# Optimization experiments

Measured on AMD Instinct MI355X. Metric: run time of the kernel, lower is better.

The kernel has to match this reference:

```python
import jax, jax.numpy as jnp
import numpy as np

TEMP = 0.1  # self._get_temperature


def _gate(cur_iter):
    return max((10000 - cur_iter) / 10000.0, 0.0)


def _vector_quantize(feat, codebook, gate):
    # feat: (b, c, h, w), codebook: (k, c)
    b, c, h, w = feat.shape
    flat = feat.transpose(0, 2, 3, 1).reshape(-1, c)  # (N, c)
    distance = (jnp.sum(flat * flat, axis=1, keepdims=True)
                + jnp.sum(codebook * codebook, axis=1)
                - 2.0 * jnp.matmul(flat, codebook.T))  # (N, k)
    prob = jax.nn.softmax(-distance / TEMP, axis=-1)  # (N, k)
    assignment = prob.reshape(b, h, w, -1).transpose(0, 3, 1, 2)  # (b, k, h, w)
    q_feat = jnp.matmul(prob, codebook).reshape(b, h, w, c).transpose(0, 3, 1, 2)
    out_feat = feat * gate + q_feat * (1.0 - gate)
    return out_feat, assignment, distance


def _head(x, w1, b1, w2, b2):
    # two 1x1 convs with ReLU in between
    y = jnp.einsum('bchw,oc->bohw', x, w1) + b1[None, :, None, None]
    y = jax.nn.relu(y)
    y = jnp.einsum('bchw,oc->bohw', y, w2) + b2[None, :, None, None]
    return y


def setup_inputs() -> dict:
    key = jax.random.key(0)
    ks = jax.random.split(key, 6)
    B, C, H, W = 32, 64, 40, 40
    K0, C1 = 2048, 256
    K1 = 512
    return {
        'x0': jax.random.normal(ks[0], (B, C, H, W), dtype=jnp.float32),
        'vq0': jax.random.normal(ks[1], (K0, C), dtype=jnp.float32),
        'vq1': jax.random.normal(ks[2], (K1, C1), dtype=jnp.float32),
        'head_w1': jax.random.normal(ks[3], (C1, C), dtype=jnp.float32) * 0.05,
        'head_b1': jnp.zeros((C1,), dtype=jnp.float32),
        'head_w2': jax.random.normal(ks[4], (C1, C1), dtype=jnp.float32) * 0.05,
        'head_b2': jnp.zeros((C1,), dtype=jnp.float32),
        'cur_iter': 5000,
    }


def reference(x0, vq0, vq1, head_w1, head_b1, head_w2, head_b2, cur_iter):
    gate = _gate(cur_iter)
    qx0, a0, d0 = _vector_quantize(x0, vq0, gate)
    x3 = _head(qx0, head_w1, head_b1, head_w2, head_b2)
    qx3, a3, d3 = _vector_quantize(x3, vq1, gate)
    # mirrors torch forward return: ([x0, x3], [qx0, qx3], [a0, a3], [d0, d3])
    return (x3, qx0, qx3, a0, a3, d0, d3)
```

## Files before the change

kernel.cpp:

```cpp
#include <hip/hip_runtime.h>
#include <math.h>

#define HW   1600
#define C0   64
#define K0   2048
#define C1   256
#define K1   512

static const size_t OFF_X3  = 0;
static const size_t OFF_QX0 = 13107200;
static const size_t OFF_QX3 = 16384000;
static const size_t OFF_A0  = 29491200;
static const size_t OFF_A3  = 134348800;
static const size_t OFF_D0  = 160563200;
static const size_t OFF_D3  = 265420800;

__global__ __launch_bounds__(256) void k_esq(const float* __restrict__ vq0,
                                             const float* __restrict__ vq1,
                                             float* __restrict__ esq) {
    int r = blockIdx.x * 256 + threadIdx.x;
    if (r < K0) {
        float s = 0.f;
        for (int c = 0; c < C0; c++) { float v = vq0[r * C0 + c]; s += v * v; }
        esq[r] = s;
    } else if (r < K0 + K1) {
        int rr = r - K0;
        float s = 0.f;
        for (int c = 0; c < C1; c++) { float v = vq1[rr * C1 + c]; s += v * v; }
        esq[K0 + rr] = s;
    }
}

__global__ __launch_bounds__(256) void k_dist0(const float* __restrict__ x0,
                                               const float* __restrict__ cb,
                                               const float* __restrict__ esq,
                                               float* __restrict__ d0,
                                               float* __restrict__ stats) {
    __shared__ __align__(16) float xs[32][68];
    __shared__ float xsq[32];
    __shared__ __align__(16) float esT[64][132];
    __shared__ float rowM[32], rowS[32];

    const int t = threadIdx.x;
    const int n0 = blockIdx.x * 32;
    const int b = n0 / HW, hw0 = n0 % HW;

    for (int i = t; i < 32 * 64; i += 256) {
        int c = i >> 5, r = i & 31;
        xs[r][c] = x0[(size_t)(b * C0 + c) * HW + hw0 + r];
    }
    __syncthreads();
    if (t < 32) {
        float s = 0.f;
        for (int c = 0; c < 64; c++) { float v = xs[t][c]; s += v * v; }
        xsq[t] = s; rowM[t] = -1e30f; rowS[t] = 0.f;
    }
    __syncthreads();

    const int rg = t >> 5;
    const int kg = t & 31;

    for (int k0 = 0; k0 < K0; k0 += 128) {
        for (int i = t; i < 128 * 64; i += 256) {
            int c = i & 63, kk = i >> 6;
            esT[c][kk] = cb[(size_t)(k0 + kk) * C0 + c];
        }
        __syncthreads();

        float acc[4][4];
        #pragma unroll
        for (int i = 0; i < 4; i++)
            #pragma unroll
            for (int j = 0; j < 4; j++) acc[i][j] = 0.f;

        #pragma unroll 2
        for (int c = 0; c < 64; c += 4) {
            float xv[4][4];
            #pragma unroll
            for (int i = 0; i < 4; i++) {
                float4 xt = *(const float4*)&xs[rg * 4 + i][c];
                xv[i][0] = xt.x; xv[i][1] = xt.y; xv[i][2] = xt.z; xv[i][3] = xt.w;
            }
            #pragma unroll
            for (int q = 0; q < 4; q++) {
                float4 ev = *(const float4*)&esT[c + q][kg * 4];
                #pragma unroll
                for (int i = 0; i < 4; i++) {
                    acc[i][0] += xv[i][q] * ev.x;
                    acc[i][1] += xv[i][q] * ev.y;
                    acc[i][2] += xv[i][q] * ev.z;
                    acc[i][3] += xv[i][q] * ev.w;
                }
            }
        }

        float4 eq = *(const float4*)&esq[k0 + kg * 4];
        float eqv[4] = {eq.x, eq.y, eq.z, eq.w};
        float mrow[4], srow[4];
        #pragma unroll
        for (int i = 0; i < 4; i++) {
            int r = rg * 4 + i;
            float xq = xsq[r];
            float dv[4];
            #pragma unroll
            for (int j = 0; j < 4; j++) dv[j] = xq + eqv[j] - 2.f * acc[i][j];
            float4 st; st.x = dv[0]; st.y = dv[1]; st.z = dv[2]; st.w = dv[3];
            *(float4*)&d0[(size_t)(n0 + r) * K0 + k0 + kg * 4] = st;
            float m = -10.f * dv[0];
            m = fmaxf(m, -10.f * dv[1]);
            m = fmaxf(m, -10.f * dv[2]);
            m = fmaxf(m, -10.f * dv[3]);
            float s = 0.f;
            #pragma unroll
            for (int j = 0; j < 4; j++) s += __expf(-10.f * dv[j] - m);
            mrow[i] = m; srow[i] = s;
        }
        #pragma unroll
        for (int off = 1; off < 32; off <<= 1) {
            #pragma unroll
            for (int i = 0; i < 4; i++) {
                float m2 = __shfl_xor(mrow[i], off, 64);
                float s2 = __shfl_xor(srow[i], off, 64);
                float M = fmaxf(mrow[i], m2);
                srow[i] = srow[i] * __expf(mrow[i] - M) + s2 * __expf(m2 - M);
                mrow[i] = M;
            }
        }
        if (kg == 0) {
            #pragma unroll
            for (int i = 0; i < 4; i++) {
                int r = rg * 4 + i;
                float Mo = rowM[r], So = rowS[r];
                float M = fmaxf(Mo, mrow[i]);
                rowS[r] = So * __expf(Mo - M) + srow[i] * __expf(mrow[i] - M);
                rowM[r] = M;
            }
        }
        __syncthreads();
    }
    if (t < 32) {
        stats[(size_t)(n0 + t) * 2]     = rowM[t];
        stats[(size_t)(n0 + t) * 2 + 1] = rowS[t];
    }
}

__global__ __launch_bounds__(256) void k_prob0(const float* __restrict__ x0,
                                               const float* __restrict__ cb,
                                               const float* __restrict__ stats,
                                               const int* __restrict__ iter,
                                               const float* __restrict__ d0,
                                               float* __restrict__ out) {
    __shared__ __align__(16) float es[128][68];
    __shared__ float ptT[128][33];
    __shared__ float rowMv[32], rowIS[32];

    const int t = threadIdx.x;
    const int n0 = blockIdx.x * 32;
    const int b = n0 / HW, hw0 = n0 % HW;

    if (t < 32) {
        rowMv[t] = stats[(size_t)(n0 + t) * 2];
        rowIS[t] = 1.f / stats[(size_t)(n0 + t) * 2 + 1];
    }
    __syncthreads();

    const int r1 = t >> 3;
    const int ks1 = (t & 7) * 16;
    const int rq = t & 31;
    const int cg = t >> 5;
    const float Mr1 = rowMv[r1], IS1 = rowIS[r1];

    float qf[8];
    #pragma unroll
    for (int q = 0; q < 8; q++) qf[q] = 0.f;

    float* a0 = out + OFF_A0;

    for (int k0 = 0; k0 < K0; k0 += 128) {
        for (int i = t; i < 128 * 64; i += 256) {
            int kk = i >> 6, c = i & 63;
            es[kk][c] = cb[(size_t)(k0 + kk) * C0 + c];
        }
        const float* dr = &d0[(size_t)(n0 + r1) * K0 + k0 + ks1];
        #pragma unroll
        for (int q = 0; q < 4; q++) {
            float4 dv = *(const float4*)&dr[q * 4];
            ptT[ks1 + q * 4 + 0][r1] = __expf(-10.f * dv.x - Mr1) * IS1;
            ptT[ks1 + q * 4 + 1][r1] = __expf(-10.f * dv.y - Mr1) * IS1;
            ptT[ks1 + q * 4 + 2][r1] = __expf(-10.f * dv.z - Mr1) * IS1;
            ptT[ks1 + q * 4 + 3][r1] = __expf(-10.f * dv.w - Mr1) * IS1;
        }
        __syncthreads();
        #pragma unroll
        for (int jj = 0; jj < 16; jj++) {
            int pos = jj * 256 + t;
            int kk = pos >> 5, r = pos & 31;
            a0[(size_t)(b * K0 + k0 + kk) * HW + hw0 + r] = ptT[kk][r];
        }
        #pragma unroll 8
        for (int kk = 0; kk < 128; kk++) {
            float p = ptT[kk][rq];
            float4 e0 = *(const float4*)&es[kk][cg * 8];
            float4 e1 = *(const float4*)&es[kk][cg * 8 + 4];
            qf[0] += p * e0.x; qf[1] += p * e0.y; qf[2] += p * e0.z; qf[3] += p * e0.w;
            qf[4] += p * e1.x; qf[5] += p * e1.y; qf[6] += p * e1.z; qf[7] += p * e1.w;
        }
        __syncthreads();
    }
    float gate = fmaxf((10000.f - (float)(*iter)) / 10000.f, 0.f);
    float om = 1.f - gate;
    #pragma unroll
    for (int q = 0; q < 8; q++) {
        int c = cg * 8 + q;
        size_t idx = (size_t)(b * C0 + c) * HW + hw0 + rq;
        out[OFF_QX0 + idx] = gate * x0[idx] + om * qf[q];
    }
}

__global__ __launch_bounds__(256) void k_head(const float* __restrict__ w1,
                                              const float* __restrict__ b1,
                                              const float* __restrict__ w2,
                                              const float* __restrict__ b2,
                                              float* __restrict__ out) {
    __shared__ __align__(16) float xin[32][64];
    __shared__ __align__(16) float y1s[32][256];
    __shared__ __align__(16) float wst[64][68];

    const int t = threadIdx.x;
    const int n0 = blockIdx.x * 32;
    const int b = n0 / HW, hw0 = n0 % HW;
    const float* qx0 = out + OFF_QX0;
    float* x3 = out + OFF_X3;

    for (int i = t; i < 32 * 64; i += 256) {
        int c = i >> 5, r = i & 31;
        xin[r][c] = qx0[(size_t)(b * C0 + c) * HW + hw0 + r];
    }
    __syncthreads();

    const int rg = t >> 5;
    const int og = t & 31;

    for (int op = 0; op < 4; op++) {
        int ob = op * 64;
        for (int i = t; i < 64 * 64; i += 256) {
            int c = i & 63, o = i >> 6;
            wst[c][o] = w1[(size_t)(ob + o) * C0 + c];
        }
        __syncthreads();
        float2 bb = *(const float2*)&b1[ob + og * 2];
        float acc[4][2];
        #pragma unroll
        for (int i = 0; i < 4; i++) { acc[i][0] = bb.x; acc[i][1] = bb.y; }
        #pragma unroll 2
        for (int c = 0; c < 64; c += 4) {
            float xv[4][4];
            #pragma unroll
            for (int i = 0; i < 4; i++) {
                float4 xt = *(const float4*)&xin[rg * 4 + i][c];
                xv[i][0] = xt.x; xv[i][1] = xt.y; xv[i][2] = xt.z; xv[i][3] = xt.w;
            }
            #pragma unroll
            for (int q = 0; q < 4; q++) {
                float2 wv = *(const float2*)&wst[c + q][og * 2];
                #pragma unroll
                for (int i = 0; i < 4; i++) {
                    acc[i][0] += xv[i][q] * wv.x;
                    acc[i][1] += xv[i][q] * wv.y;
                }
            }
        }
        #pragma unroll
        for (int i = 0; i < 4; i++) {
            float2 st;
            st.x = fmaxf(acc[i][0], 0.f);
            st.y = fmaxf(acc[i][1], 0.f);
            *(float2*)&y1s[rg * 4 + i][ob + og * 2] = st;
        }
        __syncthreads();
    }

    for (int p = 0; p < 4; p++) {
        int ob = p * 64;
        float2 bb = *(const float2*)&b2[ob + og * 2];
        float acc[4][2];
        #pragma unroll
        for (int i = 0; i < 4; i++) { acc[i][0] = bb.x; acc[i][1] = bb.y; }
        for (int cc0 = 0; cc0 < 256; cc0 += 64) {
            for (int i = t; i < 64 * 64; i += 256) {
                int c = i & 63, o = i >> 6;
                wst[c][o] = w2[(size_t)(ob + o) * C1 + cc0 + c];
            }
            __syncthreads();
            #pragma unroll 2
            for (int c = 0; c < 64; c += 4) {
                float yv[4][4];
                #pragma unroll
                for (int i = 0; i < 4; i++) {
                    float4 yt = *(const float4*)&y1s[rg * 4 + i][cc0 + c];
                    yv[i][0] = yt.x; yv[i][1] = yt.y; yv[i][2] = yt.z; yv[i][3] = yt.w;
                }
                #pragma unroll
                for (int q = 0; q < 4; q++) {
                    float2 wv = *(const float2*)&wst[c + q][og * 2];
                    #pragma unroll
                    for (int i = 0; i < 4; i++) {
                        acc[i][0] += yv[i][q] * wv.x;
                        acc[i][1] += yv[i][q] * wv.y;
                    }
                }
            }
            __syncthreads();
        }
        #pragma unroll
        for (int i = 0; i < 4; i++)
            *(float2*)&wst[0][0 + (size_t)(rg * 4 + i) * 68 + og * 2] =
                make_float2(acc[i][0], acc[i][1]);
        __syncthreads();
        for (int i = t; i < 32 * 64; i += 256) {
            int o = i >> 5, r = i & 31;
            x3[(size_t)(b * C1 + ob + o) * HW + hw0 + r] = wst[0][(size_t)r * 68 + o];
        }
        __syncthreads();
    }
}

__global__ __launch_bounds__(256) void k_dist1(const float* __restrict__ cb,
                                               const float* __restrict__ esq,
                                               const float* __restrict__ x3,
                                               float* __restrict__ d3,
                                               float* __restrict__ stats) {
    __shared__ __align__(16) float xs[32][132];
    __shared__ float esT[128][33];
    __shared__ float xsq[32];
    __shared__ float part[32][8];
    __shared__ float rowM[32], rowS[32];

    const int t = threadIdx.x;
    const int n0 = blockIdx.x * 32;
    const int b = n0 / HW, hw0 = n0 % HW;

    {
        int r = t & 31, seg = t >> 5;
        float s = 0.f;
        for (int j = 0; j < 32; j++) {
            float v = x3[(size_t)(b * C1 + seg * 32 + j) * HW + hw0 + r];
            s += v * v;
        }
        part[r][seg] = s;
    }
    __syncthreads();
    if (t < 32) {
        float s = 0.f;
        for (int j = 0; j < 8; j++) s += part[t][j];
        xsq[t] = s; rowM[t] = -1e30f; rowS[t] = 0.f;
    }
    __syncthreads();

    const int rg = t >> 5;
    const int kg = t & 31;

    for (int k0 = 0; k0 < K1; k0 += 32) {
        float acc[4] = {0.f, 0.f, 0.f, 0.f};
        for (int ch = 0; ch < 2; ch++) {
            for (int i = t; i < 32 * 128; i += 256) {
                int c = i & 127, kk = i >> 7;
                esT[c][kk] = cb[(size_t)(k0 + kk) * C1 + ch * 128 + c];
            }
            for (int i = t; i < 32 * 128; i += 256) {
                int ci = i >> 5, r = i & 31;
                xs[r][ci] = x3[(size_t)(b * C1 + ch * 128 + ci) * HW + hw0 + r];
            }
            __syncthreads();
            #pragma unroll 2
            for (int c = 0; c < 128; c += 4) {
                float ev[4];
                #pragma unroll
                for (int q = 0; q < 4; q++) ev[q] = esT[c + q][kg];
                #pragma unroll
                for (int i = 0; i < 4; i++) {
                    float4 xt = *(const float4*)&xs[rg * 4 + i][c];
                    acc[i] += xt.x * ev[0] + xt.y * ev[1] + xt.z * ev[2] + xt.w * ev[3];
                }
            }
            __syncthreads();
        }
        float eqv = esq[k0 + kg];
        float mrow[4], srow[4];
        #pragma unroll
        for (int i = 0; i < 4; i++) {
            int r = rg * 4 + i;
            float dv = xsq[r] + eqv - 2.f * acc[i];
            d3[(size_t)(n0 + r) * K1 + k0 + kg] = dv;
            mrow[i] = -10.f * dv; srow[i] = 1.f;
        }
        #pragma unroll
        for (int off = 1; off < 32; off <<= 1) {
            #pragma unroll
            for (int i = 0; i < 4; i++) {
                float m2 = __shfl_xor(mrow[i], off, 64);
                float s2 = __shfl_xor(srow[i], off, 64);
                float M = fmaxf(mrow[i], m2);
                srow[i] = srow[i] * __expf(mrow[i] - M) + s2 * __expf(m2 - M);
                mrow[i] = M;
            }
        }
        if (kg == 0) {
            #pragma unroll
            for (int i = 0; i < 4; i++) {
                int r = rg * 4 + i;
                float Mo = rowM[r], So = rowS[r];
                float M = fmaxf(Mo, mrow[i]);
                rowS[r] = So * __expf(Mo - M) + srow[i] * __expf(mrow[i] - M);
                rowM[r] = M;
            }
        }
    }
    __syncthreads();
    if (t < 32) {
        stats[(size_t)(n0 + t) * 2]     = rowM[t];
        stats[(size_t)(n0 + t) * 2 + 1] = rowS[t];
    }
}

__global__ __launch_bounds__(256) void k_prob1(const float* __restrict__ cb,
                                               const float* __restrict__ stats,
                                               const int* __restrict__ iter,
                                               const float* __restrict__ d3,
                                               float* __restrict__ out) {
    __shared__ __align__(16) float es[64][132];
    __shared__ float ptT[64][33];
    __shared__ float rowMv[32], rowIS[32];

    const int t = threadIdx.x;
    const int n0 = blockIdx.x * 32;
    const int b = n0 / HW, hw0 = n0 % HW;

    if (t < 32) {
        rowMv[t] = stats[(size_t)(n0 + t) * 2];
        rowIS[t] = 1.f / stats[(size_t)(n0 + t) * 2 + 1];
    }
    __syncthreads();

    const int r1 = t >> 3;
    const int ks1 = (t & 7) * 8;
    const int rq = t & 31;
    const int cg = t >> 5;
    const float Mr1 = rowMv[r1], IS1 = rowIS[r1];

    float qf[2][16];
    #pragma unroll
    for (int ch = 0; ch < 2; ch++)
        #pragma unroll
        for (int q = 0; q < 16; q++) qf[ch][q] = 0.f;

    const float* x3 = out + OFF_X3;
    float* a3 = out + OFF_A3;

    for (int k0 = 0; k0 < K1; k0 += 64) {
        const float* dr = &d3[(size_t)(n0 + r1) * K1 + k0 + ks1];
        float4 dv0 = *(const float4*)&dr[0];
        float4 dv1 = *(const float4*)&dr[4];
        ptT[ks1 + 0][r1] = __expf(-10.f * dv0.x - Mr1) * IS1;
        ptT[ks1 + 1][r1] = __expf(-10.f * dv0.y - Mr1) * IS1;
        ptT[ks1 + 2][r1] = __expf(-10.f * dv0.z - Mr1) * IS1;
        ptT[ks1 + 3][r1] = __expf(-10.f * dv0.w - Mr1) * IS1;
        ptT[ks1 + 4][r1] = __expf(-10.f * dv1.x - Mr1) * IS1;
        ptT[ks1 + 5][r1] = __expf(-10.f * dv1.y - Mr1) * IS1;
        ptT[ks1 + 6][r1] = __expf(-10.f * dv1.z - Mr1) * IS1;
        ptT[ks1 + 7][r1] = __expf(-10.f * dv1.w - Mr1) * IS1;
        for (int i = t; i < 64 * 128; i += 256) {
            int c = i & 127, kk = i >> 7;
            es[kk][c] = cb[(size_t)(k0 + kk) * C1 + c];
        }
        __syncthreads();
        #pragma unroll
        for (int jj = 0; jj < 8; jj++) {
            int pos = jj * 256 + t;
            int kk = pos >> 5, r = pos & 31;
            a3[(size_t)(b * K1 + k0 + kk) * HW + hw0 + r] = ptT[kk][r];
        }
        #pragma unroll 4
        for (int kk = 0; kk < 64; kk++) {
            float p = ptT[kk][rq];
            #pragma unroll
            for (int q = 0; q < 4; q++) {
                float4 e = *(const float4*)&es[kk][cg * 16 + q * 4];
                qf[0][q * 4 + 0] += p * e.x;
                qf[0][q * 4 + 1] += p * e.y;
                qf[0][q * 4 + 2] += p * e.z;
                qf[0][q * 4 + 3] += p * e.w;
            }
        }
        __syncthreads();
        for (int i = t; i < 64 * 128; i += 256) {
            int c = i & 127, kk = i >> 7;
            es[kk][c] = cb[(size_t)(k0 + kk) * C1 + 128 + c];
        }
        __syncthreads();
        #pragma unroll 4
        for (int kk = 0; kk < 64; kk++) {
            float p = ptT[kk][rq];
            #pragma unroll
            for (int q = 0; q < 4; q++) {
                float4 e = *(const float4*)&es[kk][cg * 16 + q * 4];
                qf[1][q * 4 + 0] += p * e.x;
                qf[1][q * 4 + 1] += p * e.y;
                qf[1][q * 4 + 2] += p * e.z;
                qf[1][q * 4 + 3] += p * e.w;
            }
        }
        __syncthreads();
    }
    float gate = fmaxf((10000.f - (float)(*iter)) / 10000.f, 0.f);
    float om = 1.f - gate;
    #pragma unroll
    for (int ch = 0; ch < 2; ch++) {
        #pragma unroll
        for (int q = 0; q < 16; q++) {
            int c = ch * 128 + cg * 16 + q;
            size_t idx = (size_t)(b * C1 + c) * HW + hw0 + rq;
            out[OFF_QX3 + idx] = gate * x3[idx] + om * qf[ch][q];
        }
    }
}

extern "C" void kernel_launch(void* const* d_in, const int* in_sizes, int n_in,
                              void* d_out, int out_size, void* d_ws, size_t ws_size,
                              hipStream_t stream) {
    (void)in_sizes; (void)n_in; (void)out_size; (void)ws_size;
    const float* x0  = (const float*)d_in[0];
    const float* vq0 = (const float*)d_in[1];
    const float* vq1 = (const float*)d_in[2];
    const float* w1  = (const float*)d_in[3];
    const float* b1  = (const float*)d_in[4];
    const float* w2  = (const float*)d_in[5];
    const float* b2  = (const float*)d_in[6];
    const int*   it  = (const int*)d_in[7];
    float* out = (float*)d_out;
    float* ws  = (float*)d_ws;
    float* esq0   = ws;
    float* esq1   = ws + 2048;
    float* stats0 = ws + 2560;
    float* stats1 = ws + 2560 + 2 * 51200;

    hipLaunchKernelGGL(k_esq,   dim3(10),   dim3(256), 0, stream, vq0, vq1, ws);
    hipLaunchKernelGGL(k_dist0, dim3(1600), dim3(256), 0, stream, x0, vq0, esq0,
                       out + OFF_D0, stats0);
    hipLaunchKernelGGL(k_prob0, dim3(1600), dim3(256), 0, stream, x0, vq0, stats0, it,
                       out + OFF_D0, out);
    hipLaunchKernelGGL(k_head,  dim3(1600), dim3(256), 0, stream, w1, b1, w2, b2, out);
    hipLaunchKernelGGL(k_dist1, dim3(1600), dim3(256), 0, stream, vq1, esq1,
                       out + OFF_X3, out + OFF_D3, stats1);
    hipLaunchKernelGGL(k_prob1, dim3(1600), dim3(256), 0, stream, vq1, stats1, it,
                       out + OFF_D3, out);
}
```

Before: 2.728 ms.

## Retile VQ distance/prob kernels, per-thread online softmax, exp2, prefetch, swizzled LDS

Doubles the row tile of the first-stage distance and probability kernels to 64 rows per block and halves their grid. The online softmax state now lives in per-thread registers and is reduced across lanes once at the end, replacing a shuffle reduction and LDS update on every k-tile. Exponentials switch to exp2 with a pre-scaled constant. Other changes: XOR-swizzled LDS layout for the transposed codebook, float4 codebook loads, register prefetch of the next distance tile, and staging the full 256-channel x3 tile once in k_dist1. The larger tiles raise register and LDS use, which may lower occupancy.

```diff
diff --git a/kernel.cpp b/kernel.cpp
--- a/kernel.cpp
+++ b/kernel.cpp
@@ -6,6 +6,7 @@
 #define K0   2048
 #define C1   256
 #define K1   512
+#define C2E  (-14.42695040888963f)
 
 static const size_t OFF_X3  = 0;
 static const size_t OFF_QX0 = 13107200;
@@ -36,111 +37,114 @@
                                                const float* __restrict__ esq,
                                                float* __restrict__ d0,
                                                float* __restrict__ stats) {
-    __shared__ __align__(16) float xs[32][68];
-    __shared__ float xsq[32];
+    __shared__ __align__(16) float xs[64][68];
     __shared__ __align__(16) float esT[64][132];
-    __shared__ float rowM[32], rowS[32];
+    __shared__ float part[64][4];
+    __shared__ float xsq[64];
 
     const int t = threadIdx.x;
-    const int n0 = blockIdx.x * 32;
+    const int n0 = blockIdx.x * 64;
     const int b = n0 / HW, hw0 = n0 % HW;
 
-    for (int i = t; i < 32 * 64; i += 256) {
-        int c = i >> 5, r = i & 31;
+    for (int i = t; i < 64 * 64; i += 256) {
+        int c = i >> 6, r = i & 63;
         xs[r][c] = x0[(size_t)(b * C0 + c) * HW + hw0 + r];
     }
     __syncthreads();
-    if (t < 32) {
+    {
+        int r = t & 63, seg = t >> 6;
         float s = 0.f;
-        for (int c = 0; c < 64; c++) { float v = xs[t][c]; s += v * v; }
-        xsq[t] = s; rowM[t] = -1e30f; rowS[t] = 0.f;
-    }
+        #pragma unroll
+        for (int j = 0; j < 16; j++) { float v = xs[r][seg * 16 + j]; s += v * v; }
+        part[r][seg] = s;
+    }
+    __syncthreads();
+    if (t < 64) xsq[t] = part[t][0] + part[t][1] + part[t][2] + part[t][3];
     __syncthreads();
 
     const int rg = t >> 5;
     const int kg = t & 31;
 
+    float m2r[8], sr[8];
+    #pragma unroll
+    for (int i = 0; i < 8; i++) { m2r[i] = -3.0e38f; sr[i] = 0.f; }
+
     for (int k0 = 0; k0 < K0; k0 += 128) {
-        for (int i = t; i < 128 * 64; i += 256) {
-            int c = i & 63, kk = i >> 6;
-            esT[c][kk] = cb[(size_t)(k0 + kk) * C0 + c];
-        }
-        __syncthreads();
-
-        float acc[4][4];
-        #pragma unroll
-        for (int i = 0; i < 4; i++)
+        for (int i = t; i < 2048; i += 256) {
+            int c4 = i & 15, kk = i >> 4;
+            float4 e = *(const float4*)&cb[(size_t)(k0 + kk) * C0 + c4 * 4];
+            int col = (((kk >> 2) ^ (c4 & 7)) << 2) | (kk & 3);
+            esT[c4 * 4 + 0][col] = e.x;
+            esT[c4 * 4 + 1][col] = e.y;
+            esT[c4 * 4 + 2][col] = e.z;
+            esT[c4 * 4 + 3][col] = e.w;
+        }
+        __syncthreads();
+
+        float acc[8][4];
+        #pragma unroll
+        for (int i = 0; i < 8; i++)
             #pragma unroll
             for (int j = 0; j < 4; j++) acc[i][j] = 0.f;
 
         #pragma unroll 2
         for (int c = 0; c < 64; c += 4) {
-            float xv[4][4];
-            #pragma unroll
-            for (int i = 0; i < 4; i++) {
-                float4 xt = *(const float4*)&xs[rg * 4 + i][c];
-                xv[i][0] = xt.x; xv[i][1] = xt.y; xv[i][2] = xt.z; xv[i][3] = xt.w;
-            }
-            #pragma unroll
-            for (int q = 0; q < 4; q++) {
-                float4 ev = *(const float4*)&esT[c + q][kg * 4];
-                #pragma unroll
-                for (int i = 0; i < 4; i++) {
-                    acc[i][0] += xv[i][q] * ev.x;
-                    acc[i][1] += xv[i][q] * ev.y;
-                    acc[i][2] += xv[i][q] * ev.z;
-                    acc[i][3] += xv[i][q] * ev.w;
-                }
+            int kgf = ((kg ^ ((c >> 2) & 7)) << 2);
+            float4 e0 = *(const float4*)&esT[c + 0][kgf];
+            float4 e1 = *(const float4*)&esT[c + 1][kgf];
+            float4 e2 = *(const float4*)&esT[c + 2][kgf];
+            float4 e3 = *(const float4*)&esT[c + 3][kgf];
+            #pragma unroll
+            for (int i = 0; i < 8; i++) {
+                float4 xt = *(const float4*)&xs[rg * 8 + i][c];
+                acc[i][0] += xt.x * e0.x + xt.y * e1.x + xt.z * e2.x + xt.w * e3.x;
+                acc[i][1] += xt.x * e0.y + xt.y * e1.y + xt.z * e2.y + xt.w * e3.y;
+                acc[i][2] += xt.x * e0.z + xt.y * e1.z + xt.z * e2.z + xt.w * e3.z;
+                acc[i][3] += xt.x * e0.w + xt.y * e1.w + xt.z * e2.w + xt.w * e3.w;
             }
         }
 
         float4 eq = *(const float4*)&esq[k0 + kg * 4];
-        float eqv[4] = {eq.x, eq.y, eq.z, eq.w};
-        float mrow[4], srow[4];
-        #pragma unroll
-        for (int i = 0; i < 4; i++) {
-            int r = rg * 4 + i;
+        #pragma unroll
+        for (int i = 0; i < 8; i++) {
+            int r = rg * 8 + i;
             float xq = xsq[r];
-            float dv[4];
-            #pragma unroll
-            for (int j = 0; j < 4; j++) dv[j] = xq + eqv[j] - 2.f * acc[i][j];
-            float4 st; st.x = dv[0]; st.y = dv[1]; st.z = dv[2]; st.w = dv[3];
+            float d0v = (xq + eq.x) - 2.f * acc[i][0];
+            float d1v = (xq + eq.y) - 2.f * acc[i][1];
+            float d2v = (xq + eq.z) - 2.f * acc[i][2];
+            float d3v = (xq + eq.w) - 2.f * acc[i][3];
+            float4 st; st.x = d0v; st.y = d1v; st.z = d2v; st.w = d3v;
             *(float4*)&d0[(size_t)(n0 + r) * K0 + k0 + kg * 4] = st;
-            float m = -10.f * dv[0];
-            m = fmaxf(m, -10.f * dv[1]);
-            m = fmaxf(m, -10.f * dv[2]);
-            m = fmaxf(m, -10.f * dv[3]);
-            float s = 0.f;
-            #pragma unroll
-            for (int j = 0; j < 4; j++) s += __expf(-10.f * dv[j] - m);
-            mrow[i] = m; srow[i] = s;
-        }
-        #pragma unroll
-        for (int off = 1; off < 32; off <<= 1) {
-            #pragma unroll
-            for (int i = 0; i < 4; i++) {
-                float m2 = __shfl_xor(mrow[i], off, 64);
-                float s2 = __shfl_xor(srow[i], off, 64);
-                float M = fmaxf(mrow[i], m2);
-                srow[i] = srow[i] * __expf(mrow[i] - M) + s2 * __expf(m2 - M);
-                mrow[i] = M;
-            }
-        }
-        if (kg == 0) {
-            #pragma unroll
-            for (int i = 0; i < 4; i++) {
-                int r = rg * 4 + i;
-                float Mo = rowM[r], So = rowS[r];
-                float M = fmaxf(Mo, mrow[i]);
-                rowS[r] = So * __expf(Mo - M) + srow[i] * __expf(mrow[i] - M);
-                rowM[r] = M;
-            }
-        }
-        __syncthreads();
-    }
-    if (t < 32) {
-        stats[(size_t)(n0 + t) * 2]     = rowM[t];
-        stats[(size_t)(n0 + t) * 2 + 1] = rowS[t];
+            float p0 = C2E * d0v, p1 = C2E * d1v, p2 = C2E * d2v, p3 = C2E * d3v;
+            float mm = fmaxf(fmaxf(p0, p1), fmaxf(p2, p3));
+            float Mn = fmaxf(m2r[i], mm);
+            float ss = __builtin_amdgcn_exp2f(p0 - Mn) + __builtin_amdgcn_exp2f(p1 - Mn)
+                     + __builtin_amdgcn_exp2f(p2 - Mn) + __builtin_amdgcn_exp2f(p3 - Mn);
+            sr[i] = sr[i] * __builtin_amdgcn_exp2f(m2r[i] - Mn) + ss;
+            m2r[i] = Mn;
+        }
+        __syncthreads();
+    }
+
+    #pragma unroll
+    for (int off = 1; off < 32; off <<= 1) {
+        #pragma unroll
+        for (int i = 0; i < 8; i++) {
+            float m2 = __shfl_xor(m2r[i], off, 64);
+            float s2 = __shfl_xor(sr[i], off, 64);
+            float Mn = fmaxf(m2r[i], m2);
+            sr[i] = sr[i] * __builtin_amdgcn_exp2f(m2r[i] - Mn)
+                  + s2 * __builtin_amdgcn_exp2f(m2 - Mn);
+            m2r[i] = Mn;
+        }
+    }
+    if (kg == 0) {
+        #pragma unroll
+        for (int i = 0; i < 8; i++) {
+            int r = rg * 8 + i;
+            stats[(size_t)(n0 + r) * 2]     = m2r[i];
+            stats[(size_t)(n0 + r) * 2 + 1] = sr[i];
+        }
     }
 }
 
@@ -151,67 +155,84 @@
                                                const float* __restrict__ d0,
                                                float* __restrict__ out) {
     __shared__ __align__(16) float es[128][68];
-    __shared__ float ptT[128][33];
-    __shared__ float rowMv[32], rowIS[32];
+    __shared__ float ptT[128][66];
+    __shared__ float rowM[64], rowIS[64];
 
     const int t = threadIdx.x;
-    const int n0 = blockIdx.x * 32;
+    const int n0 = blockIdx.x * 64;
     const int b = n0 / HW, hw0 = n0 % HW;
 
-    if (t < 32) {
-        rowMv[t] = stats[(size_t)(n0 + t) * 2];
+    if (t < 64) {
+        rowM[t]  = stats[(size_t)(n0 + t) * 2];
         rowIS[t] = 1.f / stats[(size_t)(n0 + t) * 2 + 1];
     }
     __syncthreads();
 
-    const int r1 = t >> 3;
-    const int ks1 = (t & 7) * 16;
-    const int rq = t & 31;
-    const int cg = t >> 5;
-    const float Mr1 = rowMv[r1], IS1 = rowIS[r1];
-
-    float qf[8];
-    #pragma unroll
-    for (int q = 0; q < 8; q++) qf[q] = 0.f;
+    const int r1 = t >> 2;
+    const int ks1 = (t & 3) * 32;
+    const int rq = t & 63;
+    const int cg = t >> 6;
+    const float Mr1 = rowM[r1], IS1 = rowIS[r1];
+
+    float qf[16];
+    #pragma unroll
+    for (int q = 0; q < 16; q++) qf[q] = 0.f;
 
     float* a0 = out + OFF_A0;
 
+    float4 dpre[8];
+    {
+        const float* dr = &d0[(size_t)(n0 + r1) * K0 + ks1];
+        #pragma unroll
+        for (int q = 0; q < 8; q++) dpre[q] = *(const float4*)&dr[q * 4];
+    }
+
     for (int k0 = 0; k0 < K0; k0 += 128) {
-        for (int i = t; i < 128 * 64; i += 256) {
-            int kk = i >> 6, c = i & 63;
-            es[kk][c] = cb[(size_t)(k0 + kk) * C0 + c];
-        }
-        const float* dr = &d0[(size_t)(n0 + r1) * K0 + k0 + ks1];
-        #pragma unroll
-        for (int q = 0; q < 4; q++) {
-            float4 dv = *(const float4*)&dr[q * 4];
-            ptT[ks1 + q * 4 + 0][r1] = __expf(-10.f * dv.x - Mr1) * IS1;
-            ptT[ks1 + q * 4 + 1][r1] = __expf(-10.f * dv.y - Mr1) * IS1;
-            ptT[ks1 + q * 4 + 2][r1] = __expf(-10.f * dv.z - Mr1) * IS1;
-            ptT[ks1 + q * 4 + 3][r1] = __expf(-10.f * dv.w - Mr1) * IS1;
-        }
-        __syncthreads();
-        #pragma unroll
-        for (int jj = 0; jj < 16; jj++) {
+        for (int i = t; i < 2048; i += 256) {
+            int c4 = i & 15, kk = i >> 4;
+            *(float4*)&es[kk][c4 * 4] =
+                *(const float4*)&cb[(size_t)(k0 + kk) * C0 + c4 * 4];
+        }
+        #pragma unroll
+        for (int q = 0; q < 8; q++) {
+            float4 dv = dpre[q];
+            int kb = ks1 + q * 4;
+            ptT[kb + 0][r1] = __builtin_amdgcn_exp2f(C2E * dv.x - Mr1) * IS1;
+            ptT[kb + 1][r1] = __builtin_amdgcn_exp2f(C2E * dv.y - Mr1) * IS1;
+            ptT[kb + 2][r1] = __builtin_amdgcn_exp2f(C2E * dv.z - Mr1) * IS1;
+            ptT[kb + 3][r1] = __builtin_amdgcn_exp2f(C2E * dv.w - Mr1) * IS1;
+        }
+        if (k0 + 128 < K0) {
+            const float* dr = &d0[(size_t)(n0 + r1) * K0 + k0 + 128 + ks1];
+            #pragma unroll
+            for (int q = 0; q < 8; q++) dpre[q] = *(const float4*)&dr[q * 4];
+        }
+        __syncthreads();
+        #pragma unroll
+        for (int jj = 0; jj < 32; jj++) {
             int pos = jj * 256 + t;
-            int kk = pos >> 5, r = pos & 31;
+            int kk = pos >> 6, r = pos & 63;
             a0[(size_t)(b * K0 + k0 + kk) * HW + hw0 + r] = ptT[kk][r];
         }
         #pragma unroll 8
         for (int kk = 0; kk < 128; kk++) {
             float p = ptT[kk][rq];
-            float4 e0 = *(const float4*)&es[kk][cg * 8];
-            float4 e1 = *(const float4*)&es[kk][cg * 8 + 4];
-            qf[0] += p * e0.x; qf[1] += p * e0.y; qf[2] += p * e0.z; qf[3] += p * e0.w;
-            qf[4] += p * e1.x; qf[5] += p * e1.y; qf[6] += p * e1.z; qf[7] += p * e1.w;
+            float4 e0 = *(const float4*)&es[kk][cg * 16];
+            float4 e1 = *(const float4*)&es[kk][cg * 16 + 4];
+            float4 e2 = *(const float4*)&es[kk][cg * 16 + 8];
+            float4 e3 = *(const float4*)&es[kk][cg * 16 + 12];
+            qf[0]  += p * e0.x; qf[1]  += p * e0.y; qf[2]  += p * e0.z; qf[3]  += p * e0.w;
+            qf[4]  += p * e1.x; qf[5]  += p * e1.y; qf[6]  += p * e1.z; qf[7]  += p * e1.w;
+            qf[8]  += p * e2.x; qf[9]  += p * e2.y; qf[10] += p * e2.z; qf[11] += p * e2.w;
+            qf[12] += p * e3.x; qf[13] += p * e3.y; qf[14] += p * e3.z; qf[15] += p * e3.w;
         }
         __syncthreads();
     }
     float gate = fmaxf((10000.f - (float)(*iter)) / 10000.f, 0.f);
     float om = 1.f - gate;
     #pragma unroll
-    for (int q = 0; q < 8; q++) {
-        int c = cg * 8 + q;
+    for (int q = 0; q < 16; q++) {
+        int c = cg * 16 + q;
         size_t idx = (size_t)(b * C0 + c) * HW + hw0 + rq;
         out[OFF_QX0 + idx] = gate * x0[idx] + om * qf[q];
     }
@@ -330,96 +351,97 @@
                                                const float* __restrict__ x3,
                                                float* __restrict__ d3,
                                                float* __restrict__ stats) {
-    __shared__ __align__(16) float xs[32][132];
-    __shared__ float esT[128][33];
+    __shared__ __align__(16) float xs[32][260];
+    __shared__ float esT[256][37];
+    __shared__ float part[32][8];
     __shared__ float xsq[32];
-    __shared__ float part[32][8];
-    __shared__ float rowM[32], rowS[32];
 
     const int t = threadIdx.x;
     const int n0 = blockIdx.x * 32;
     const int b = n0 / HW, hw0 = n0 % HW;
 
+    for (int i = t; i < 32 * 256; i += 256) {
+        int ci = i >> 5, r = i & 31;
+        xs[r][ci] = x3[(size_t)(b * C1 + ci) * HW + hw0 + r];
+    }
+    __syncthreads();
     {
         int r = t & 31, seg = t >> 5;
         float s = 0.f;
-        for (int j = 0; j < 32; j++) {
-            float v = x3[(size_t)(b * C1 + seg * 32 + j) * HW + hw0 + r];
-            s += v * v;
-        }
+        #pragma unroll
+        for (int j = 0; j < 32; j++) { float v = xs[r][seg * 32 + j]; s += v * v; }
         part[r][seg] = s;
     }
     __syncthreads();
     if (t < 32) {
         float s = 0.f;
+        #pragma unroll
         for (int j = 0; j < 8; j++) s += part[t][j];
-        xsq[t] = s; rowM[t] = -1e30f; rowS[t] = 0.f;
+        xsq[t] = s;
     }
     __syncthreads();
 
     const int rg = t >> 5;
     const int kg = t & 31;
 
+    float m2r[4], sr[4];
+    #pragma unroll
+    for (int i = 0; i < 4; i++) { m2r[i] = -3.0e38f; sr[i] = 0.f; }
+
     for (int k0 = 0; k0 < K1; k0 += 32) {
+        for (int i = t; i < 32 * 256; i += 256) {
+            int c = i & 255, kk = i >> 8;
+            esT[c][kk] = cb[(size_t)(k0 + kk) * C1 + c];
+        }
+        __syncthreads();
+
         float acc[4] = {0.f, 0.f, 0.f, 0.f};
-        for (int ch = 0; ch < 2; ch++) {
-            for (int i = t; i < 32 * 128; i += 256) {
-                int c = i & 127, kk = i >> 7;
-                esT[c][kk] = cb[(size_t)(k0 + kk) * C1 + ch * 128 + c];
-            }
-            for (int i = t; i < 32 * 128; i += 256) {
-                int ci = i >> 5, r = i & 31;
-                xs[r][ci] = x3[(size_t)(b * C1 + ch * 128 + ci) * HW + hw0 + r];
-            }
-            __syncthreads();
-            #pragma unroll 2
-            for (int c = 0; c < 128; c += 4) {
-                float ev[4];
-                #pragma unroll
-                for (int q = 0; q < 4; q++) ev[q] = esT[c + q][kg];
-                #pragma unroll
-                for (int i = 0; i < 4; i++) {
-                    float4 xt = *(const float4*)&xs[rg * 4 + i][c];
-                    acc[i] += xt.x * ev[0] + xt.y * ev[1] + xt.z * ev[2] + xt.w * ev[3];
-                }
-            }
-            __syncthreads();
+        #pragma unroll 2
+        for (int c = 0; c < 256; c += 4) {
+            float e0 = esT[c + 0][kg];
+            float e1 = esT[c + 1][kg];
+            float e2 = esT[c + 2][kg];
+            float e3 = esT[c + 3][kg];
+            #pragma unroll
+            for (int i = 0; i < 4; i++) {
+                float4 xt = *(const float4*)&xs[rg * 4 + i][c];
+                acc[i] += xt.x * e0 + xt.y * e1 + xt.z * e2 + xt.w * e3;
+            }
         }
         float eqv = esq[k0 + kg];
-        float mrow[4], srow[4];
         #pragma unroll
         for (int i = 0; i < 4; i++) {
             int r = rg * 4 + i;
-            float dv = xsq[r] + eqv - 2.f * acc[i];
+            float dv = (xsq[r] + eqv) - 2.f * acc[i];
             d3[(size_t)(n0 + r) * K1 + k0 + kg] = dv;
-            mrow[i] = -10.f * dv; srow[i] = 1.f;
-        }
-        #pragma unroll
-        for (int off = 1; off < 32; off <<= 1) {
-            #pragma unroll
-            for (int i = 0; i < 4; i++) {
-                float m2 = __shfl_xor(mrow[i], off, 64);
-                float s2 = __shfl_xor(srow[i], off, 64);
-                float M = fmaxf(mrow[i], m2);
-                srow[i] = srow[i] * __expf(mrow[i] - M) + s2 * __expf(m2 - M);
-                mrow[i] = M;
-            }
-        }
-        if (kg == 0) {
-            #pragma unroll
-            for (int i = 0; i < 4; i++) {
-                int r = rg * 4 + i;
-                float Mo = rowM[r], So = rowS[r];
-                float M = fmaxf(Mo, mrow[i]);
-                rowS[r] = So * __expf(Mo - M) + srow[i] * __expf(mrow[i] - M);
-                rowM[r] = M;
-            }
-        }
-    }
-    __syncthreads();
-    if (t < 32) {
-        stats[(size_t)(n0 + t) * 2]     = rowM[t];
-        stats[(size_t)(n0 + t) * 2 + 1] = rowS[t];
+            float p = C2E * dv;
+            float Mn = fmaxf(m2r[i], p);
+            sr[i] = sr[i] * __builtin_amdgcn_exp2f(m2r[i] - Mn)
+                  + __builtin_amdgcn_exp2f(p - Mn);
+            m2r[i] = Mn;
+        }
+        __syncthreads();
+    }
+
+    #pragma unroll
+    for (int off = 1; off < 32; off <<= 1) {
+        #pragma unroll
+        for (int i = 0; i < 4; i++) {
+            float m2 = __shfl_xor(m2r[i], off, 64);
+            float s2 = __shfl_xor(sr[i], off, 64);
+            float Mn = fmaxf(m2r[i], m2);
+            sr[i] = sr[i] * __builtin_amdgcn_exp2f(m2r[i] - Mn)
+                  + s2 * __builtin_amdgcn_exp2f(m2 - Mn);
+            m2r[i] = Mn;
+        }
+    }
+    if (kg == 0) {
+        #pragma unroll
+        for (int i = 0; i < 4; i++) {
+            int r = rg * 4 + i;
+            stats[(size_t)(n0 + r) * 2]     = m2r[i];
+            stats[(size_t)(n0 + r) * 2 + 1] = sr[i];
+        }
     }
 }
 
@@ -430,14 +452,14 @@
                                                float* __restrict__ out) {
     __shared__ __align__(16) float es[64][132];
     __shared__ float ptT[64][33];
-    __shared__ float rowMv[32], rowIS[32];
+    __shared__ float rowM[32], rowIS[32];
 
     const int t = threadIdx.x;
     const int n0 = blockIdx.x * 32;
     const int b = n0 / HW, hw0 = n0 % HW;
 
     if (t < 32) {
-        rowMv[t] = stats[(size_t)(n0 + t) * 2];
+        rowM[t]  = stats[(size_t)(n0 + t) * 2];
         rowIS[t] = 1.f / stats[(size_t)(n0 + t) * 2 + 1];
     }
     __syncthreads();
@@ -446,32 +468,43 @@
     const int ks1 = (t & 7) * 8;
     const int rq = t & 31;
     const int cg = t >> 5;
-    const float Mr1 = rowMv[r1], IS1 = rowIS[r1];
-
-    float qf[2][16];
-    #pragma unroll
-    for (int ch = 0; ch < 2; ch++)
-        #pragma unroll
-        for (int q = 0; q < 16; q++) qf[ch][q] = 0.f;
+    const float Mr1 = rowM[r1], IS1 = rowIS[r1];
+
+    float qf0[16], qf1[16];
+    #pragma unroll
+    for (int q = 0; q < 16; q++) { qf0[q] = 0.f; qf1[q] = 0.f; }
 
     const float* x3 = out + OFF_X3;
     float* a3 = out + OFF_A3;
 
+    float4 dpre0, dpre1;
+    {
+        const float* dr = &d3[(size_t)(n0 + r1) * K1 + ks1];
+        dpre0 = *(const float4*)&dr[0];
+        dpre1 = *(const float4*)&dr[4];
+    }
+
     for (int k0 = 0; k0 < K1; k0 += 64) {
-        const float* dr = &d3[(size_t)(n0 + r1) * K1 + k0 + ks1];
-        float4 dv0 = *(const float4*)&dr[0];
-        float4 dv1 = *(const float4*)&dr[4];
-        ptT[ks1 + 0][r1] = __expf(-10.f * dv0.x - Mr1) * IS1;
-        ptT[ks1 + 1][r1] = __expf(-10.f * dv0.y - Mr1) * IS1;
-        ptT[ks1 + 2][r1] = __expf(-10.f * dv0.z - Mr1) * IS1;
-        ptT[ks1 + 3][r1] = __expf(-10.f * dv0.w - Mr1) * IS1;
-        ptT[ks1 + 4][r1] = __expf(-10.f * dv1.x - Mr1) * IS1;
-        ptT[ks1 + 5][r1] = __expf(-10.f * dv1.y - Mr1) * IS1;
-        ptT[ks1 + 6][r1] = __expf(-10.f * dv1.z - Mr1) * IS1;
-        ptT[ks1 + 7][r1] = __expf(-10.f * dv1.w - Mr1) * IS1;
-        for (int i = t; i < 64 * 128; i += 256) {
-            int c = i & 127, kk = i >> 7;
-            es[kk][c] = cb[(size_t)(k0 + kk) * C1 + c];
+        {
+            float4 v0 = dpre0, v1 = dpre1;
+            ptT[ks1 + 0][r1] = __builtin_amdgcn_exp2f(C2E * v0.x - Mr1) * IS1;
+            ptT[ks1 + 1][r1] = __builtin_amdgcn_exp2f(C2E * v0.y - Mr1) * IS1;
+            ptT[ks1 + 2][r1] = __builtin_amdgcn_exp2f(C2E * v0.z - Mr1) * IS1;
+            ptT[ks1 + 3][r1] = __builtin_amdgcn_exp2f(C2E * v0.w - Mr1) * IS1;
+            ptT[ks1 + 4][r1] = __builtin_amdgcn_exp2f(C2E * v1.x - Mr1) * IS1;
+            ptT[ks1 + 5][r1] = __builtin_amdgcn_exp2f(C2E * v1.y - Mr1) * IS1;
+            ptT[ks1 + 6][r1] = __builtin_amdgcn_exp2f(C2E * v1.z - Mr1) * IS1;
+            ptT[ks1 + 7][r1] = __builtin_amdgcn_exp2f(C2E * v1.w - Mr1) * IS1;
+        }
+        if (k0 + 64 < K1) {
+            const float* dr = &d3[(size_t)(n0 + r1) * K1 + k0 + 64 + ks1];
+            dpre0 = *(const float4*)&dr[0];
+            dpre1 = *(const float4*)&dr[4];
+        }
+        for (int i = t; i < 2048; i += 256) {
+            int c4 = i & 31, kk = i >> 5;
+            *(float4*)&es[kk][c4 * 4] =
+                *(const float4*)&cb[(size_t)(k0 + kk) * C1 + c4 * 4];
         }
         __syncthreads();
         #pragma unroll
@@ -486,16 +519,17 @@
             #pragma unroll
             for (int q = 0; q < 4; q++) {
                 float4 e = *(const float4*)&es[kk][cg * 16 + q * 4];
-                qf[0][q * 4 + 0] += p * e.x;
-                qf[0][q * 4 + 1] += p * e.y;
-                qf[0][q * 4 + 2] += p * e.z;
-                qf[0][q * 4 + 3] += p * e.w;
-            }
-        }
-        __syncthreads();
-        for (int i = t; i < 64 * 128; i += 256) {
-            int c = i & 127, kk = i >> 7;
-            es[kk][c] = cb[(size_t)(k0 + kk) * C1 + 128 + c];
+                qf0[q * 4 + 0] += p * e.x;
+                qf0[q * 4 + 1] += p * e.y;
+                qf0[q * 4 + 2] += p * e.z;
+                qf0[q * 4 + 3] += p * e.w;
+            }
+        }
+        __syncthreads();
+        for (int i = t; i < 2048; i += 256) {
+            int c4 = i & 31, kk = i >> 5;
+            *(float4*)&es[kk][c4 * 4] =
+                *(const float4*)&cb[(size_t)(k0 + kk) * C1 + 128 + c4 * 4];
         }
         __syncthreads();
         #pragma unroll 4
@@ -504,10 +538,10 @@
             #pragma unroll
             for (int q = 0; q < 4; q++) {
                 float4 e = *(const float4*)&es[kk][cg * 16 + q * 4];
-                qf[1][q * 4 + 0] += p * e.x;
-                qf[1][q * 4 + 1] += p * e.y;
-                qf[1][q * 4 + 2] += p * e.z;
-                qf[1][q * 4 + 3] += p * e.w;
+                qf1[q * 4 + 0] += p * e.x;
+                qf1[q * 4 + 1] += p * e.y;
+                qf1[q * 4 + 2] += p * e.z;
+                qf1[q * 4 + 3] += p * e.w;
             }
         }
         __syncthreads();
@@ -515,13 +549,16 @@
     float gate = fmaxf((10000.f - (float)(*iter)) / 10000.f, 0.f);
     float om = 1.f - gate;
     #pragma unroll
-    for (int ch = 0; ch < 2; ch++) {
-        #pragma unroll
-        for (int q = 0; q < 16; q++) {
-            int c = ch * 128 + cg * 16 + q;
-            size_t idx = (size_t)(b * C1 + c) * HW + hw0 + rq;
-            out[OFF_QX3 + idx] = gate * x3[idx] + om * qf[ch][q];
-        }
+    for (int q = 0; q < 16; q++) {
+        int c = cg * 16 + q;
+        size_t idx = (size_t)(b * C1 + c) * HW + hw0 + rq;
+        out[OFF_QX3 + idx] = gate * x3[idx] + om * qf0[q];
+    }
+    #pragma unroll
+    for (int q = 0; q < 16; q++) {
+        int c = 128 + cg * 16 + q;
+        size_t idx = (size_t)(b * C1 + c) * HW + hw0 + rq;
+        out[OFF_QX3 + idx] = gate * x3[idx] + om * qf1[q];
     }
 }
 
@@ -545,9 +582,9 @@
     float* stats1 = ws + 2560 + 2 * 51200;
 
     hipLaunchKernelGGL(k_esq,   dim3(10),   dim3(256), 0, stream, vq0, vq1, ws);
-    hipLaunchKernelGGL(k_dist0, dim3(1600), dim3(256), 0, stream, x0, vq0, esq0,
+    hipLaunchKernelGGL(k_dist0, dim3(800),  dim3(256), 0, stream, x0, vq0, esq0,
                        out + OFF_D0, stats0);
-    hipLaunchKernelGGL(k_prob0, dim3(1600), dim3(256), 0, stream, x0, vq0, stats0, it,
+    hipLaunchKernelGGL(k_prob0, dim3(800),  dim3(256), 0, stream, x0, vq0, stats0, it,
                        out + OFF_D0, out);
     hipLaunchKernelGGL(k_head,  dim3(1600), dim3(256), 0, stream, w1, b1, w2, b2, out);
     hipLaunchKernelGGL(k_dist1, dim3(1600), dim3(256), 0, stream, vq1, esq1,
```

Result: slower. 2.990 ms (+9.6%).
